# Kernel optimization log

Measured on AMD Instinct MI355X. Metric: run time of the kernel, lower is better.

Reference implementation:

```python
import jax, jax.numpy as jnp
import numpy as np

N_NODES = 100000
N_EDGES = 1280000
D_IN = 64
D_OUT = 64


def setup_inputs() -> dict:
    key = jax.random.key(0)
    k_x, k_e, k_w, k_rw = jax.random.split(key, 4)
    x = jax.random.normal(k_x, (N_NODES, D_IN), dtype=jnp.float32)
    edge_index = jax.random.randint(k_e, (2, N_EDGES), 0, N_NODES, dtype=jnp.int32)
    glorot = float(np.sqrt(6.0 / (D_IN + D_OUT)))
    weight = jax.random.uniform(k_w, (D_IN, D_OUT), dtype=jnp.float32, minval=-glorot, maxval=glorot)
    root_weight = jax.random.uniform(k_rw, (D_IN, D_OUT), dtype=jnp.float32, minval=-glorot, maxval=glorot)
    bias = jnp.zeros((D_OUT,), dtype=jnp.float32)
    return {"x": x, "edge_index": edge_index, "weight": weight,
            "root_weight": root_weight, "bias": bias}


def reference(x, edge_index, weight, root_weight, bias):
    # adj_0 = SparseTensor(row=edge_index[0], col=edge_index[1])
    # adj_0.matmul(x, reduce='mean'): out[i] = mean_{(i,j) in E} x[j]
    n = x.shape[0]
    row, col = edge_index[0], edge_index[1]
    msg = x[col]                                              # [E, D_in] gather
    summed = jax.ops.segment_sum(msg, row, num_segments=n)    # [N, D_in]
    count = jax.ops.segment_sum(jnp.ones((row.shape[0],), dtype=x.dtype), row,
                                num_segments=n)               # [N]
    agg = summed / jnp.maximum(count, 1.0)[:, None]           # mean (deg-0 -> 0)
    out = agg @ weight + x @ root_weight + bias
    return out
```

## Files before the change

kernel.cpp:

```cpp
#include <hip/hip_runtime.h>
#include <hip/hip_bf16.h>

#define N_NODES 100000
#define N_EDGES 1280000
#define D 64
#define NB ((N_NODES + 255) / 256)
#define NBKT 391
#define BKT_SHIFT 8
#define BKT_NODES 256
#define CAP 3712
#define COL_PAD 4096
#define BIN_EPB 4096

using short8 = __attribute__((ext_vector_type(8))) short;
using f32x4  = __attribute__((ext_vector_type(4))) float;

__device__ __forceinline__ unsigned short f2bf(float f) {
    unsigned int u = __float_as_uint(f);
    unsigned int r = (u + 0x7FFFu + ((u >> 16) & 1u)) >> 16;
    return (unsigned short)r;
}

__device__ __forceinline__ float bf2f(unsigned short u) {
    union { unsigned int i; float f; } v;
    v.i = ((unsigned int)u) << 16;
    return v.f;
}


__global__ void bin_kernel(const int* __restrict__ row,
                           const int* __restrict__ col,
                           int* __restrict__ bucket_cnt,
                           unsigned int* __restrict__ pairs) {
    __shared__ int cnt[NBKT];
    __shared__ int gbase[NBKT];
    __shared__ int lcur[NBKT];

    int tid = threadIdx.x;
    for (int i = tid; i < NBKT; i += 256) { cnt[i] = 0; lcur[i] = 0; }
    __syncthreads();

    int rr[16], cc[16];
#pragma unroll
    for (int i = 0; i < 16; ++i) {
        int e = blockIdx.x * BIN_EPB + i * 256 + tid;
        if (e < N_EDGES) {
            rr[i] = row[e];
            cc[i] = col[e];
            atomicAdd(&cnt[rr[i] >> BKT_SHIFT], 1);
        } else {
            rr[i] = -1;
        }
    }
    __syncthreads();
    for (int i = tid; i < NBKT; i += 256)
        if (cnt[i] > 0) gbase[i] = atomicAdd(&bucket_cnt[i], cnt[i]);
    __syncthreads();

#pragma unroll
    for (int i = 0; i < 16; ++i) {
        if (rr[i] >= 0) {
            int b = rr[i] >> BKT_SHIFT;
            int slot = gbase[b] + atomicAdd(&lcur[b], 1);
            if (slot < CAP)
                pairs[(size_t)b * CAP + slot] =
                    ((unsigned int)(rr[i] & (BKT_NODES - 1)) << 17) | (unsigned int)cc[i];
        }
    }
}

__global__ void precompute_kernel(const float* __restrict__ x,
                                  const float* __restrict__ W,
                                  const float* __restrict__ Wr,
                                  const float* __restrict__ bias,
                                  unsigned int* __restrict__ y_packed,
                                  float* __restrict__ out) {
    __shared__ unsigned short Wl[8192];

    int tid = threadIdx.x;
    for (int idx = tid; idx < 8192; idx += 256) {
        int j    = idx & 7;
        int lane = (idx >> 3) & 63;
        int h    = (idx >> 9) & 1;
        int t    = (idx >> 10) & 3;
        int mat  = idx >> 12;
        int k = h * 32 + ((lane >> 4) << 3) + j;
        int n = t * 16 + (lane & 15);
        const float* src = mat ? Wr : W;
        Wl[idx] = f2bf(src[k * D + n]);
    }
    __syncthreads();

    int wv = tid >> 6;
    int lane = tid & 63;
    int g = blockIdx.x * 4 + wv;
    if (g >= N_NODES / 16) return;

    int quad = lane >> 4;
    int n16 = lane & 15;
    int m_node = g * 16 + n16;

    short8 A[2];
#pragma unroll
    for (int h = 0; h < 2; ++h) {
        const float* xr = x + (size_t)m_node * D + h * 32 + quad * 8;
        float4 xa = *(const float4*)xr;
        float4 xb = *(const float4*)(xr + 4);
        short8 a;
        a[0] = (short)f2bf(xa.x); a[1] = (short)f2bf(xa.y);
        a[2] = (short)f2bf(xa.z); a[3] = (short)f2bf(xa.w);
        a[4] = (short)f2bf(xb.x); a[5] = (short)f2bf(xb.y);
        a[6] = (short)f2bf(xb.z); a[7] = (short)f2bf(xb.w);
        A[h] = a;
    }

    int row0 = g * 16 + quad * 4;

#pragma unroll
    for (int t = 0; t < 4; ++t) {
        short8 By0 = *(const short8*)&Wl[(((0 * 4 + t) * 2 + 0) * 64 + lane) * 8];
        short8 By1 = *(const short8*)&Wl[(((0 * 4 + t) * 2 + 1) * 64 + lane) * 8];
        short8 Bz0 = *(const short8*)&Wl[(((1 * 4 + t) * 2 + 0) * 64 + lane) * 8];
        short8 Bz1 = *(const short8*)&Wl[(((1 * 4 + t) * 2 + 1) * 64 + lane) * 8];

        f32x4 accY = {0.f, 0.f, 0.f, 0.f};
        accY = __builtin_amdgcn_mfma_f32_16x16x32_bf16(A[0], By0, accY, 0, 0, 0);
        accY = __builtin_amdgcn_mfma_f32_16x16x32_bf16(A[1], By1, accY, 0, 0, 0);
        f32x4 accZ = {0.f, 0.f, 0.f, 0.f};
        accZ = __builtin_amdgcn_mfma_f32_16x16x32_bf16(A[0], Bz0, accZ, 0, 0, 0);
        accZ = __builtin_amdgcn_mfma_f32_16x16x32_bf16(A[1], Bz1, accZ, 0, 0, 0);

        float bv = bias[t * 16 + n16];
#pragma unroll
        for (int r = 0; r < 4; ++r) {
            out[(size_t)(row0 + r) * D + t * 16 + n16] = accZ[r] + bv;
            unsigned int me = f2bf(accY[r]);
            unsigned int nb = (unsigned int)__shfl_xor((int)me, 1, 64) & 0xFFFFu;
            if ((lane & 1) == 0)
                y_packed[((size_t)(row0 + r) * D + t * 16 + n16) >> 1] = me | (nb << 16);
        }
    }
}

__launch_bounds__(1024, 8)
__global__ void csr_gather_kernel(const unsigned short* __restrict__ yu,
                                  const unsigned int* __restrict__ pairs,
                                  const int* __restrict__ bucket_cnt,
                                  float* __restrict__ out) {
    __shared__ int col_lds[COL_PAD];
    __shared__ int deg_s[BKT_NODES];
    __shared__ int start_s[BKT_NODES];
    __shared__ int lcur[BKT_NODES];
    __shared__ int cnt_s[BKT_NODES];
    __shared__ int wsum[4];

    int b = blockIdx.x;
    int tid = threadIdx.x;
    int m = bucket_cnt[b];
    if (m > CAP) m = CAP;
    const unsigned int* pb = pairs + (size_t)b * CAP;

    if (tid < BKT_NODES) cnt_s[tid] = 0;
    __syncthreads();

    uint4 p4 = ((const uint4*)pb)[tid];
    bool v0 = (4 * tid + 0) < m, v1 = (4 * tid + 1) < m,
         v2 = (4 * tid + 2) < m, v3 = (4 * tid + 3) < m;
    if (v0) atomicAdd(&cnt_s[p4.x >> 17], 1);
    if (v1) atomicAdd(&cnt_s[p4.y >> 17], 1);
    if (v2) atomicAdd(&cnt_s[p4.z >> 17], 1);
    if (v3) atomicAdd(&cnt_s[p4.w >> 17], 1);
    __syncthreads();

    if (tid < BKT_NODES) {
        int v = cnt_s[tid];
        int incl = v;
        for (int d = 1; d < 64; d <<= 1) {
            int t = __shfl_up(incl, d, 64);
            if ((tid & 63) >= d) incl += t;
        }
        if ((tid & 63) == 63) wsum[tid >> 6] = incl;
        deg_s[tid] = v;
        cnt_s[tid] = incl;
    }
    __syncthreads();
    if (tid < BKT_NODES) {
        int w = tid >> 6;
        int pre = 0;
        if (w > 0) pre += wsum[0];
        if (w > 1) pre += wsum[1];
        if (w > 2) pre += wsum[2];
        int excl = cnt_s[tid] + pre - deg_s[tid];
        start_s[tid] = excl;
        lcur[tid] = excl;
    }
    __syncthreads();

    if (v0) { int r = (int)(p4.x >> 17); int c = (int)(p4.x & 0x1FFFFu);
              col_lds[atomicAdd(&lcur[r], 1)] = c < N_NODES ? c : 0; }
    if (v1) { int r = (int)(p4.y >> 17); int c = (int)(p4.y & 0x1FFFFu);
              col_lds[atomicAdd(&lcur[r], 1)] = c < N_NODES ? c : 0; }
    if (v2) { int r = (int)(p4.z >> 17); int c = (int)(p4.z & 0x1FFFFu);
              col_lds[atomicAdd(&lcur[r], 1)] = c < N_NODES ? c : 0; }
    if (v3) { int r = (int)(p4.w >> 17); int c = (int)(p4.w & 0x1FFFFu);
              col_lds[atomicAdd(&lcur[r], 1)] = c < N_NODES ? c : 0; }
    __syncthreads();

    int wv = tid >> 6;
    int lane = tid & 63;
    int s = lane >> 4;
    int q = lane & 15;

#pragma unroll 1
    for (int pk = 0; pk < 4; ++pk) {
        int n0 = wv * 16 + pk * 4;
        int nvx = deg_s[n0 + 0], nvy = deg_s[n0 + 1],
            nvz = deg_s[n0 + 2], nvw = deg_s[n0 + 3];
        int st0 = start_s[n0 + 0], st1 = start_s[n0 + 1],
            st2 = start_s[n0 + 2], st3 = start_s[n0 + 3];

        float4 a0 = make_float4(0.f, 0.f, 0.f, 0.f);
        float4 a1 = a0, a2 = a0, a3 = a0;

        {
            int mm = nvx > nvy ? nvx : nvy;
            for (int j = 0; j < mm; j += 4) {
                int jj = j + s;
                int c0 = col_lds[(st0 + jj) & (COL_PAD - 1)];
                int c1 = col_lds[(st1 + jj) & (COL_PAD - 1)];
                c0 = (jj < nvx) ? c0 : 0;
                c1 = (jj < nvy) ? c1 : 0;
                ushort4 u0 = *(const ushort4*)&yu[(size_t)c0 * D + q * 4];
                ushort4 u1 = *(const ushort4*)&yu[(size_t)c1 * D + q * 4];
                if (jj < nvx) {
                    a0.x += bf2f(u0.x); a0.y += bf2f(u0.y);
                    a0.z += bf2f(u0.z); a0.w += bf2f(u0.w);
                }
                if (jj < nvy) {
                    a1.x += bf2f(u1.x); a1.y += bf2f(u1.y);
                    a1.z += bf2f(u1.z); a1.w += bf2f(u1.w);
                }
            }
        }
        {
            int mm = nvz > nvw ? nvz : nvw;
            for (int j = 0; j < mm; j += 4) {
                int jj = j + s;
                int c2 = col_lds[(st2 + jj) & (COL_PAD - 1)];
                int c3 = col_lds[(st3 + jj) & (COL_PAD - 1)];
                c2 = (jj < nvz) ? c2 : 0;
                c3 = (jj < nvw) ? c3 : 0;
                ushort4 u2 = *(const ushort4*)&yu[(size_t)c2 * D + q * 4];
                ushort4 u3 = *(const ushort4*)&yu[(size_t)c3 * D + q * 4];
                if (jj < nvz) {
                    a2.x += bf2f(u2.x); a2.y += bf2f(u2.y);
                    a2.z += bf2f(u2.z); a2.w += bf2f(u2.w);
                }
                if (jj < nvw) {
                    a3.x += bf2f(u3.x); a3.y += bf2f(u3.y);
                    a3.z += bf2f(u3.z); a3.w += bf2f(u3.w);
                }
            }
        }

#define BFLY(a) \
    a.x += __shfl_xor(a.x, 16, 64); a.y += __shfl_xor(a.y, 16, 64); \
    a.z += __shfl_xor(a.z, 16, 64); a.w += __shfl_xor(a.w, 16, 64); \
    a.x += __shfl_xor(a.x, 32, 64); a.y += __shfl_xor(a.y, 32, 64); \
    a.z += __shfl_xor(a.z, 32, 64); a.w += __shfl_xor(a.w, 32, 64);
        BFLY(a0) BFLY(a1) BFLY(a2) BFLY(a3)
#undef BFLY

        float inv0 = 1.0f / (float)(nvx > 1 ? nvx : 1);
        float inv1 = 1.0f / (float)(nvy > 1 ? nvy : 1);
        float inv2 = 1.0f / (float)(nvz > 1 ? nvz : 1);
        float inv3 = 1.0f / (float)(nvw > 1 ? nvw : 1);

        float4 rr = (s == 0) ? a0 : (s == 1) ? a1 : (s == 2) ? a2 : a3;
        float invs = (s == 0) ? inv0 : (s == 1) ? inv1 : (s == 2) ? inv2 : inv3;
        int g = (b << BKT_SHIFT) + n0 + s;
        if (g < N_NODES) {
            size_t off = (size_t)g * D + q * 4;
            float4 z = *(const float4*)&out[off];
            z.x += rr.x * invs; z.y += rr.y * invs;
            z.z += rr.z * invs; z.w += rr.w * invs;
            *(float4*)&out[off] = z;
        }
    }
}


__global__ void hist_kernel(const int4* __restrict__ row4, int* __restrict__ deg) {
    int t = blockIdx.x * blockDim.x + threadIdx.x;
    if (t < N_EDGES / 4) {
        int4 r = row4[t];
        atomicAdd(&deg[r.x], 1);
        atomicAdd(&deg[r.y], 1);
        atomicAdd(&deg[r.z], 1);
        atomicAdd(&deg[r.w], 1);
    }
}

__global__ void scan_block_kernel(const int* __restrict__ deg,
                                  int* __restrict__ cursor,
                                  int* __restrict__ bsum) {
    __shared__ int s[256];
    int tid = threadIdx.x;
    int gid = blockIdx.x * 256 + tid;
    int v = (gid < N_NODES) ? deg[gid] : 0;
    s[tid] = v;
    __syncthreads();
    for (int d = 1; d < 256; d <<= 1) {
        int t = (tid >= d) ? s[tid - d] : 0;
        __syncthreads();
        s[tid] += t;
        __syncthreads();
    }
    if (gid < N_NODES) cursor[gid] = s[tid] - v;
    if (tid == 255) bsum[blockIdx.x] = s[255];
}

__global__ void add_offsets_kernel(int* __restrict__ cursor,
                                   const int* __restrict__ bsum_raw) {
    __shared__ int red[256];
    int tid = threadIdx.x;
    int b = blockIdx.x;
    int sum = 0;
    for (int i = tid; i < b; i += 256) sum += bsum_raw[i];
    red[tid] = sum;
    __syncthreads();
    for (int off = 128; off > 0; off >>= 1) {
        if (tid < off) red[tid] += red[tid + off];
        __syncthreads();
    }
    int gid = b * 256 + tid;
    if (gid < N_NODES) cursor[gid] += red[0];
}

__global__ void scatter_build_kernel(const int4* __restrict__ row4,
                                     const int4* __restrict__ col4,
                                     int* __restrict__ cursor,
                                     int* __restrict__ col_sorted) {
    int t = blockIdx.x * blockDim.x + threadIdx.x;
    if (t < N_EDGES / 4) {
        int4 r = row4[t];
        int4 c = col4[t];
        col_sorted[atomicAdd(&cursor[r.x], 1)] = c.x;
        col_sorted[atomicAdd(&cursor[r.y], 1)] = c.y;
        col_sorted[atomicAdd(&cursor[r.z], 1)] = c.z;
        col_sorted[atomicAdd(&cursor[r.w], 1)] = c.w;
    }
}

__launch_bounds__(512, 8)
__global__ void aggregate_kernel(const float* __restrict__ x,
                                 const int* __restrict__ cursor_end,
                                 const int* __restrict__ deg,
                                 const int* __restrict__ col_sorted,
                                 const float* __restrict__ W,
                                 const float* __restrict__ Wr,
                                 const float* __restrict__ bias,
                                 float* __restrict__ out) {
    __shared__ float Ws[D * D];
    __shared__ float Wrs[D * D];
    __shared__ float agg_s[8][D];
    __shared__ float x_s[8][D];

    for (int i = threadIdx.x; i < D * D / 4; i += 512) {
        ((float4*)Ws)[i]  = ((const float4*)W)[i];
        ((float4*)Wrs)[i] = ((const float4*)Wr)[i];
    }
    __syncthreads();

    int wv = threadIdx.x >> 6;
    int lane = threadIdx.x & 63;
    int s = lane >> 4;
    int q = lane & 15;
    float bf = bias[lane];

    int node0 = (blockIdx.x * 8 + wv) * 4;

#pragma unroll 1
    for (int nn = 0; nn < 4; ++nn) {
        int r = node0 + nn;
        int n = deg[r];
        int start = cursor_end[r] - n;

        float4 acc = make_float4(0.f, 0.f, 0.f, 0.f);
        for (int base = 0; base < n; base += 64) {
            int m = n - base; if (m > 64) m = 64;
            int idx = 0;
            if (lane < m) idx = col_sorted[start + base + lane];
            for (int j = 0; j < m; j += 4) {
                int jj = j + s;
                int c = __shfl(idx, jj, 64);
                if (jj < m) {
                    float4 v = *(const float4*)&x[(size_t)c * D + q * 4];
                    acc.x += v.x; acc.y += v.y; acc.z += v.z; acc.w += v.w;
                }
            }
        }
        acc.x += __shfl_xor(acc.x, 16, 64);
        acc.y += __shfl_xor(acc.y, 16, 64);
        acc.z += __shfl_xor(acc.z, 16, 64);
        acc.w += __shfl_xor(acc.w, 16, 64);
        acc.x += __shfl_xor(acc.x, 32, 64);
        acc.y += __shfl_xor(acc.y, 32, 64);
        acc.z += __shfl_xor(acc.z, 32, 64);
        acc.w += __shfl_xor(acc.w, 32, 64);

        float inv = 1.0f / (float)(n > 1 ? n : 1);
        if (lane < 16) {
            float4 a = make_float4(acc.x * inv, acc.y * inv, acc.z * inv, acc.w * inv);
            *(float4*)&agg_s[wv][q * 4] = a;
            *(float4*)&x_s[wv][q * 4] = *(const float4*)&x[(size_t)r * D + q * 4];
        }
        __builtin_amdgcn_wave_barrier();

        int f = lane;
        float o = bf;
        const float4* av = (const float4*)agg_s[wv];
        const float4* xv = (const float4*)x_s[wv];
#pragma unroll
        for (int k4 = 0; k4 < 16; ++k4) {
            float4 a = av[k4];
            float4 xx = xv[k4];
            int k = k4 * 4;
            o += a.x * Ws[(k + 0) * D + f] + xx.x * Wrs[(k + 0) * D + f];
            o += a.y * Ws[(k + 1) * D + f] + xx.y * Wrs[(k + 1) * D + f];
            o += a.z * Ws[(k + 2) * D + f] + xx.z * Wrs[(k + 2) * D + f];
            o += a.w * Ws[(k + 3) * D + f] + xx.w * Wrs[(k + 3) * D + f];
        }
        out[(size_t)r * D + f] = o;
        __builtin_amdgcn_wave_barrier();
    }
}


__global__ void zero_kernel(float* __restrict__ summed, float* __restrict__ cnt) {
    int stride = gridDim.x * blockDim.x;
    int i = blockIdx.x * blockDim.x + threadIdx.x;
    const int total = N_NODES * D;
    for (int idx = i; idx < total; idx += stride) summed[idx] = 0.0f;
    for (int idx = i; idx < N_NODES; idx += stride) cnt[idx] = 0.0f;
}

__global__ void scatter_atomic_kernel(const float* __restrict__ x,
                                      const int* __restrict__ row,
                                      const int* __restrict__ col,
                                      float* __restrict__ summed,
                                      float* __restrict__ cnt) {
    long long gid = (long long)blockIdx.x * blockDim.x + threadIdx.x;
    const long long total = (long long)N_EDGES * D;
    if (gid >= total) return;
    int e = (int)(gid >> 6);
    int f = (int)(gid & 63);
    int r = row[e];
    int c = col[e];
    atomicAdd(&summed[r * D + f], x[c * D + f]);
    if (f == 0) atomicAdd(&cnt[r], 1.0f);
}

__global__ void finish_kernel(const float* __restrict__ x,
                              const float* __restrict__ W,
                              const float* __restrict__ Wr,
                              const float* __restrict__ bias,
                              const float* __restrict__ cnt,
                              float* __restrict__ out) {
    __shared__ float agg_s[4][D];
    __shared__ float x_s[4][D];
    int lrow = threadIdx.x >> 6;
    int f = threadIdx.x & 63;
    int r = blockIdx.x * 4 + lrow;

    float c = cnt[r];
    float inv = 1.0f / fmaxf(c, 1.0f);
    agg_s[lrow][f] = out[r * D + f] * inv;
    x_s[lrow][f] = x[r * D + f];
    __syncthreads();

    float acc = bias[f];
#pragma unroll 8
    for (int k = 0; k < D; ++k) {
        acc += agg_s[lrow][k] * W[k * D + f];
        acc += x_s[lrow][k] * Wr[k * D + f];
    }
    out[r * D + f] = acc;
}


extern "C" void kernel_launch(void* const* d_in, const int* in_sizes, int n_in,
                              void* d_out, int out_size, void* d_ws, size_t ws_size,
                              hipStream_t stream) {
    const float* x    = (const float*)d_in[0];
    const int*   ei   = (const int*)d_in[1];
    const float* W    = (const float*)d_in[2];
    const float* Wr   = (const float*)d_in[3];
    const float* bias = (const float*)d_in[4];
    float* out = (float*)d_out;

    const int* row = ei;
    const int* col = ei + N_EDGES;

    const size_t t1_cnt   = 0;
    const size_t t1_pairs = 2048;
    const size_t t1_y     = 2048 + (size_t)NBKT * CAP * 4;
    const size_t t1_need  = t1_y + (size_t)N_NODES * D * 2;

    const size_t csr_bytes = (size_t)2 * N_NODES * 4 + 2048 + (size_t)N_EDGES * 4;

    if (ws_size >= t1_need) {
        char* ws = (char*)d_ws;
        int* bcnt = (int*)(ws + t1_cnt);
        unsigned int* pairs    = (unsigned int*)(ws + t1_pairs);
        unsigned int* y_packed = (unsigned int*)(ws + t1_y);

        hipMemsetAsync(bcnt, 0, 2048, stream);
        bin_kernel<<<(N_EDGES + BIN_EPB - 1) / BIN_EPB, 256, 0, stream>>>(
            row, col, bcnt, pairs);
        precompute_kernel<<<(N_NODES / 16 + 3) / 4, 256, 0, stream>>>(
            x, W, Wr, bias, y_packed, out);
        csr_gather_kernel<<<NBKT, 1024, 0, stream>>>(
            (const unsigned short*)y_packed, pairs, bcnt, out);
    } else if (ws_size >= csr_bytes) {
        char* ws = (char*)d_ws;
        int* deg        = (int*)(ws);
        int* cursor     = (int*)(ws + (size_t)1 * N_NODES * 4);
        int* bsum       = (int*)(ws + (size_t)2 * N_NODES * 4);
        int* col_sorted = (int*)(ws + (size_t)2 * N_NODES * 4 + 2048);

        hipMemsetAsync(deg, 0, (size_t)N_NODES * 4, stream);
        hist_kernel<<<(N_EDGES / 4 + 255) / 256, 256, 0, stream>>>((const int4*)row, deg);
        scan_block_kernel<<<NB, 256, 0, stream>>>(deg, cursor, bsum);
        add_offsets_kernel<<<NB, 256, 0, stream>>>(cursor, bsum);
        scatter_build_kernel<<<(N_EDGES / 4 + 255) / 256, 256, 0, stream>>>(
            (const int4*)row, (const int4*)col, cursor, col_sorted);
        aggregate_kernel<<<N_NODES / 32, 512, 0, stream>>>(x, cursor, deg, col_sorted, W, Wr, bias, out);
    } else {
        float* cnt = (float*)d_ws;
        zero_kernel<<<4096, 256, 0, stream>>>(out, cnt);
        long long total = (long long)N_EDGES * D;
        int blocks = (int)((total + 255) / 256);
        scatter_atomic_kernel<<<blocks, 256, 0, stream>>>(x, row, col, out, cnt);
        finish_kernel<<<(N_NODES + 3) / 4, 256, 0, stream>>>(x, W, Wr, bias, cnt, out);
    }
}
```

Measured before the change: 158.2 us.

## Fuse binning and precompute into one launch with LDS-sorted coalesced pair writes

Merges the edge-binning kernel and the node precompute GEMM into a single launch, with block-index ranges split between the two jobs, so they can overlap on the GPU. The binning blocks now counting-sort their edges by bucket in shared memory with a prefix scan, then copy each bucket's run to global memory using 16-lane groups, which makes the pair writes contiguous instead of scattered. The memset is also replaced by a tiny zeroing kernel. The cost is larger per-block shared memory, an extra scan and sync phase, and heterogeneous blocks that may balance unevenly.

```diff
diff --git a/kernel.cpp b/kernel.cpp
--- a/kernel.cpp
+++ b/kernel.cpp
@@ -11,6 +11,8 @@
 #define CAP 3712
 #define COL_PAD 4096
 #define BIN_EPB 4096
+#define BIN_BLOCKS 313
+#define PRE_BLOCKS 782
 
 using short8 = __attribute__((ext_vector_type(8))) short;
 using f32x4  = __attribute__((ext_vector_type(4))) float;
@@ -27,117 +29,167 @@
     return v.f;
 }
 
-
-__global__ void bin_kernel(const int* __restrict__ row,
-                           const int* __restrict__ col,
-                           int* __restrict__ bucket_cnt,
-                           unsigned int* __restrict__ pairs) {
-    __shared__ int cnt[NBKT];
-    __shared__ int gbase[NBKT];
-    __shared__ int lcur[NBKT];
-
+__global__ void zero_bcnt_kernel(int* __restrict__ bcnt) {
+    int t = threadIdx.x;
+    if (t < NBKT) bcnt[t] = 0;
+}
+
+__launch_bounds__(512)
+__global__ void bin_pre_kernel(const int* __restrict__ row,
+                               const int* __restrict__ col,
+                               int* __restrict__ bucket_cnt,
+                               unsigned int* __restrict__ pairs,
+                               const float* __restrict__ x,
+                               const float* __restrict__ W,
+                               const float* __restrict__ Wr,
+                               const float* __restrict__ bias,
+                               unsigned int* __restrict__ y_packed,
+                               float* __restrict__ out) {
+    __shared__ __align__(16) char smem[22784];
     int tid = threadIdx.x;
-    for (int i = tid; i < NBKT; i += 256) { cnt[i] = 0; lcur[i] = 0; }
-    __syncthreads();
-
-    int rr[16], cc[16];
-#pragma unroll
-    for (int i = 0; i < 16; ++i) {
-        int e = blockIdx.x * BIN_EPB + i * 256 + tid;
-        if (e < N_EDGES) {
-            rr[i] = row[e];
-            cc[i] = col[e];
-            atomicAdd(&cnt[rr[i] >> BKT_SHIFT], 1);
-        } else {
-            rr[i] = -1;
-        }
-    }
-    __syncthreads();
-    for (int i = tid; i < NBKT; i += 256)
-        if (cnt[i] > 0) gbase[i] = atomicAdd(&bucket_cnt[i], cnt[i]);
-    __syncthreads();
-
-#pragma unroll
-    for (int i = 0; i < 16; ++i) {
-        if (rr[i] >= 0) {
-            int b = rr[i] >> BKT_SHIFT;
-            int slot = gbase[b] + atomicAdd(&lcur[b], 1);
-            if (slot < CAP)
-                pairs[(size_t)b * CAP + slot] =
-                    ((unsigned int)(rr[i] & (BKT_NODES - 1)) << 17) | (unsigned int)cc[i];
-        }
-    }
-}
-
-__global__ void precompute_kernel(const float* __restrict__ x,
-                                  const float* __restrict__ W,
-                                  const float* __restrict__ Wr,
-                                  const float* __restrict__ bias,
-                                  unsigned int* __restrict__ y_packed,
-                                  float* __restrict__ out) {
-    __shared__ unsigned short Wl[8192];
-
-    int tid = threadIdx.x;
-    for (int idx = tid; idx < 8192; idx += 256) {
-        int j    = idx & 7;
-        int lane = (idx >> 3) & 63;
-        int h    = (idx >> 9) & 1;
-        int t    = (idx >> 10) & 3;
-        int mat  = idx >> 12;
-        int k = h * 32 + ((lane >> 4) << 3) + j;
-        int n = t * 16 + (lane & 15);
-        const float* src = mat ? Wr : W;
-        Wl[idx] = f2bf(src[k * D + n]);
-    }
-    __syncthreads();
-
-    int wv = tid >> 6;
-    int lane = tid & 63;
-    int g = blockIdx.x * 4 + wv;
-    if (g >= N_NODES / 16) return;
-
-    int quad = lane >> 4;
-    int n16 = lane & 15;
-    int m_node = g * 16 + n16;
-
-    short8 A[2];
-#pragma unroll
-    for (int h = 0; h < 2; ++h) {
-        const float* xr = x + (size_t)m_node * D + h * 32 + quad * 8;
-        float4 xa = *(const float4*)xr;
-        float4 xb = *(const float4*)(xr + 4);
-        short8 a;
-        a[0] = (short)f2bf(xa.x); a[1] = (short)f2bf(xa.y);
-        a[2] = (short)f2bf(xa.z); a[3] = (short)f2bf(xa.w);
-        a[4] = (short)f2bf(xb.x); a[5] = (short)f2bf(xb.y);
-        a[6] = (short)f2bf(xb.z); a[7] = (short)f2bf(xb.w);
-        A[h] = a;
-    }
-
-    int row0 = g * 16 + quad * 4;
-
-#pragma unroll
-    for (int t = 0; t < 4; ++t) {
-        short8 By0 = *(const short8*)&Wl[(((0 * 4 + t) * 2 + 0) * 64 + lane) * 8];
-        short8 By1 = *(const short8*)&Wl[(((0 * 4 + t) * 2 + 1) * 64 + lane) * 8];
-        short8 Bz0 = *(const short8*)&Wl[(((1 * 4 + t) * 2 + 0) * 64 + lane) * 8];
-        short8 Bz1 = *(const short8*)&Wl[(((1 * 4 + t) * 2 + 1) * 64 + lane) * 8];
-
-        f32x4 accY = {0.f, 0.f, 0.f, 0.f};
-        accY = __builtin_amdgcn_mfma_f32_16x16x32_bf16(A[0], By0, accY, 0, 0, 0);
-        accY = __builtin_amdgcn_mfma_f32_16x16x32_bf16(A[1], By1, accY, 0, 0, 0);
-        f32x4 accZ = {0.f, 0.f, 0.f, 0.f};
-        accZ = __builtin_amdgcn_mfma_f32_16x16x32_bf16(A[0], Bz0, accZ, 0, 0, 0);
-        accZ = __builtin_amdgcn_mfma_f32_16x16x32_bf16(A[1], Bz1, accZ, 0, 0, 0);
-
-        float bv = bias[t * 16 + n16];
-#pragma unroll
-        for (int r = 0; r < 4; ++r) {
-            out[(size_t)(row0 + r) * D + t * 16 + n16] = accZ[r] + bv;
-            unsigned int me = f2bf(accY[r]);
-            unsigned int nb = (unsigned int)__shfl_xor((int)me, 1, 64) & 0xFFFFu;
-            if ((lane & 1) == 0)
-                y_packed[((size_t)(row0 + r) * D + t * 16 + n16) >> 1] = me | (nb << 16);
+
+    if (blockIdx.x < BIN_BLOCKS) {
+        unsigned int* sorted = (unsigned int*)smem;
+        int* cnt   = (int*)(smem + 16384);
+        int* lexcl = cnt + NBKT;
+        int* lcur  = lexcl + NBKT;
+        int* gbase = lcur + NBKT;
+        int* wsum  = gbase + NBKT;
+        int* wexcl = wsum + 8;
+
+        for (int i = tid; i < NBKT; i += 512) cnt[i] = 0;
+        __syncthreads();
+
+        int rr[8], cc[8];
+#pragma unroll
+        for (int i = 0; i < 8; ++i) {
+            int e = blockIdx.x * BIN_EPB + i * 512 + tid;
+            if (e < N_EDGES) {
+                rr[i] = row[e];
+                cc[i] = col[e];
+                atomicAdd(&cnt[rr[i] >> BKT_SHIFT], 1);
+            } else {
+                rr[i] = -1;
+            }
+        }
+        __syncthreads();
+
+        int lane = tid & 63, wv = tid >> 6;
+        int v = (tid < NBKT) ? cnt[tid] : 0;
+        int incl = v;
+#pragma unroll
+        for (int d = 1; d < 64; d <<= 1) {
+            int u = __shfl_up(incl, d, 64);
+            if (lane >= d) incl += u;
+        }
+        if (lane == 63) wsum[wv] = incl;
+        __syncthreads();
+        if (tid < 8) {
+            int w = wsum[tid];
+            int p = w;
+#pragma unroll
+            for (int d = 1; d < 8; d <<= 1) {
+                int u = __shfl_up(p, d, 64);
+                if (tid >= d) p += u;
+            }
+            wexcl[tid] = p - w;
+        }
+        __syncthreads();
+        if (tid < NBKT) {
+            int excl = incl - v + wexcl[wv];
+            lexcl[tid] = excl;
+            lcur[tid]  = excl;
+            if (v > 0) gbase[tid] = atomicAdd(&bucket_cnt[tid], v);
+        }
+        __syncthreads();
+
+#pragma unroll
+        for (int i = 0; i < 8; ++i) {
+            if (rr[i] >= 0) {
+                int b = rr[i] >> BKT_SHIFT;
+                int slot = atomicAdd(&lcur[b], 1);
+                sorted[slot] = ((unsigned int)(rr[i] & (BKT_NODES - 1)) << 17)
+                             | (unsigned int)cc[i];
+            }
+        }
+        __syncthreads();
+
+        int grp = tid >> 4, l16 = tid & 15;
+        for (int bb = grp; bb < NBKT; bb += 32) {
+            int len = cnt[bb];
+            if (len == 0) continue;
+            int src = lexcl[bb];
+            int dst = gbase[bb];
+            for (int k = l16; k < len; k += 16) {
+                int gs = dst + k;
+                if (gs < CAP)
+                    pairs[(size_t)bb * CAP + gs] = sorted[src + k];
+            }
+        }
+    } else {
+        unsigned short* Wl = (unsigned short*)smem;
+
+        for (int idx = tid; idx < 8192; idx += 512) {
+            int j    = idx & 7;
+            int lane = (idx >> 3) & 63;
+            int h    = (idx >> 9) & 1;
+            int t    = (idx >> 10) & 3;
+            int mat  = idx >> 12;
+            int k = h * 32 + ((lane >> 4) << 3) + j;
+            int n = t * 16 + (lane & 15);
+            const float* src = mat ? Wr : W;
+            Wl[idx] = f2bf(src[k * D + n]);
+        }
+        __syncthreads();
+
+        int wv = tid >> 6;
+        int lane = tid & 63;
+        int g = (blockIdx.x - BIN_BLOCKS) * 8 + wv;
+        if (g >= N_NODES / 16) return;
+
+        int quad = lane >> 4;
+        int n16 = lane & 15;
+        int m_node = g * 16 + n16;
+
+        short8 A[2];
+#pragma unroll
+        for (int h = 0; h < 2; ++h) {
+            const float* xr = x + (size_t)m_node * D + h * 32 + quad * 8;
+            float4 xa = *(const float4*)xr;
+            float4 xb = *(const float4*)(xr + 4);
+            short8 a;
+            a[0] = (short)f2bf(xa.x); a[1] = (short)f2bf(xa.y);
+            a[2] = (short)f2bf(xa.z); a[3] = (short)f2bf(xa.w);
+            a[4] = (short)f2bf(xb.x); a[5] = (short)f2bf(xb.y);
+            a[6] = (short)f2bf(xb.z); a[7] = (short)f2bf(xb.w);
+            A[h] = a;
+        }
+
+        int row0 = g * 16 + quad * 4;
+
+#pragma unroll
+        for (int t = 0; t < 4; ++t) {
+            short8 By0 = *(const short8*)&Wl[(((0 * 4 + t) * 2 + 0) * 64 + lane) * 8];
+            short8 By1 = *(const short8*)&Wl[(((0 * 4 + t) * 2 + 1) * 64 + lane) * 8];
+            short8 Bz0 = *(const short8*)&Wl[(((1 * 4 + t) * 2 + 0) * 64 + lane) * 8];
+            short8 Bz1 = *(const short8*)&Wl[(((1 * 4 + t) * 2 + 1) * 64 + lane) * 8];
+
+            f32x4 accY = {0.f, 0.f, 0.f, 0.f};
+            accY = __builtin_amdgcn_mfma_f32_16x16x32_bf16(A[0], By0, accY, 0, 0, 0);
+            accY = __builtin_amdgcn_mfma_f32_16x16x32_bf16(A[1], By1, accY, 0, 0, 0);
+            f32x4 accZ = {0.f, 0.f, 0.f, 0.f};
+            accZ = __builtin_amdgcn_mfma_f32_16x16x32_bf16(A[0], Bz0, accZ, 0, 0, 0);
+            accZ = __builtin_amdgcn_mfma_f32_16x16x32_bf16(A[1], Bz1, accZ, 0, 0, 0);
+
+            float bv = bias[t * 16 + n16];
+#pragma unroll
+            for (int r = 0; r < 4; ++r) {
+                out[(size_t)(row0 + r) * D + t * 16 + n16] = accZ[r] + bv;
+                unsigned int me = f2bf(accY[r]);
+                unsigned int nb = (unsigned int)__shfl_xor((int)me, 1, 64) & 0xFFFFu;
+                if ((lane & 1) == 0)
+                    y_packed[((size_t)(row0 + r) * D + t * 16 + n16) >> 1] = me | (nb << 16);
+            }
         }
     }
 }
@@ -515,11 +567,9 @@
         unsigned int* pairs    = (unsigned int*)(ws + t1_pairs);
         unsigned int* y_packed = (unsigned int*)(ws + t1_y);
 
-        hipMemsetAsync(bcnt, 0, 2048, stream);
-        bin_kernel<<<(N_EDGES + BIN_EPB - 1) / BIN_EPB, 256, 0, stream>>>(
-            row, col, bcnt, pairs);
-        precompute_kernel<<<(N_NODES / 16 + 3) / 4, 256, 0, stream>>>(
-            x, W, Wr, bias, y_packed, out);
+        zero_bcnt_kernel<<<1, 512, 0, stream>>>(bcnt);
+        bin_pre_kernel<<<BIN_BLOCKS + PRE_BLOCKS, 512, 0, stream>>>(
+            row, col, bcnt, pairs, x, W, Wr, bias, y_packed, out);
         csr_gather_kernel<<<NBKT, 1024, 0, stream>>>(
             (const unsigned short*)y_packed, pairs, bcnt, out);
     } else if (ws_size >= csr_bytes) {
```

Measured after the change: 140.5 us. 1.13x faster.
